# Kernel optimization log

Measured on AMD Instinct MI355X. Metric: run time of the kernel, lower is better.

The kernel has to match this reference:

```python
import jax, jax.numpy as jnp
import numpy as np
from jax import lax
jax.config.update("jax_enable_x64", True)

FNV_OFF = np.int64(-3750763034362895579)
FNV_PRIME = np.int64(4294967731)
I64_MAX = np.iinfo(np.int64).max
INF = np.float32(1e38)
CHUNK = 512  # cluster-chunk size for the cdist fallback


def _pack_key(b, c, vx, vy, vz):
    # five-word FNV-1a 64-bit hash with natural int64 wraparound
    h = jnp.full(b.shape, FNV_OFF, dtype=jnp.int64)
    for w in (b, c, vx, vy, vz):
        h = (h ^ w.astype(jnp.int64)) * FNV_PRIME
    return h


def _safe_norm(x):
    s = jnp.sum(x * x, axis=1)
    n = jnp.sqrt(jnp.where(s > 0, s, 1.0))
    return jnp.where(s > 0, n, 0.0)


def setup_inputs() -> dict:
    key = jax.random.key(0)
    k1, k2, k3, k4 = jax.random.split(key, 4)
    N = 65536
    grid = jax.random.randint(k1, (N, 3), 0, 400).astype(jnp.float32)
    batch_id = jnp.sort(jax.random.randint(k2, (N,), 0, 2).astype(jnp.int64))
    label = jax.random.randint(k3, (N,), 0, 8).astype(jnp.int64)
    pred_off = jax.random.normal(k4, (N, 3), dtype=jnp.float32)
    return {"pred_off": pred_off, "grid": grid, "label": label, "batch_id": batch_id,
            "base_grid": 16, "num_cls": 8, "num_batch": 2}


def _forward(pred_off, grid, label, batch_id, base_grid, num_cls, num_batch):
    N = grid.shape[0]
    grid_f = grid.astype(jnp.float32)
    vox = jnp.floor(grid_f / base_grid).astype(jnp.int64)  # [N,3]

    # voxel_grid: bucket by (batch, voxel) -> consecutive cluster ids via unique
    ckey = ((batch_id * 1024 + vox[:, 0]) * 1024 + vox[:, 1]) * 1024 + vox[:, 2]
    _, cluster = jnp.unique(ckey, return_inverse=True, size=N, fill_value=I64_MAX)
    cluster = cluster.reshape(-1)

    # cluster stats (segment scatter-reduce, num_segments = N upper bound)
    cnt = jax.ops.segment_sum(jnp.ones((N,), jnp.float32), cluster, num_segments=N)
    cl_center = jax.ops.segment_sum(grid_f, cluster, num_segments=N) / jnp.maximum(cnt, 1.0)[:, None]
    cl_batch = jax.ops.segment_min(batch_id, cluster, num_segments=N)
    cl_lbl_lo = jax.ops.segment_min(label, cluster, num_segments=N)
    cl_lbl_hi = jax.ops.segment_max(label, cluster, num_segments=N)
    cl_vox = jax.ops.segment_min(vox, cluster, num_segments=N)
    valid_cl = cnt > 0
    pure_cl = (cl_lbl_lo == cl_lbl_hi) & valid_cl
    pure_pt = pure_cl[cluster]

    # hash table of pure clusters, sorted by key (invalid -> sentinel, sorts last)
    pk_all = jnp.where(pure_cl, _pack_key(cl_batch, cl_lbl_lo, cl_vox[:, 0], cl_vox[:, 1], cl_vox[:, 2]), I64_MAX)
    order = jnp.argsort(pk_all)
    pk_sort = pk_all[order]
    pc_sort = cl_center[order]
    ok_sort = pure_cl[order]

    # per (batch,label) global centers
    key_bl = batch_id * num_cls + label
    nbl = num_batch * num_cls
    cnt_bl = jax.ops.segment_sum(jnp.ones((N,), jnp.float32), key_bl, num_segments=nbl)
    global_c = jax.ops.segment_sum(grid_f, key_bl, num_segments=nbl) / jnp.maximum(cnt_bl, 1.0)[:, None]
    step_sign = jnp.sign(global_c[key_bl] - cl_center[cluster]).astype(jnp.int64)  # [N,3]

    # +/-1 and +/-2 voxel hash lookup (steps 1 and K+1=2)
    def probe(step):
        cv = cl_vox[cluster] + step_sign * step
        ck = _pack_key(batch_id, label, cv[:, 0], cv[:, 1], cv[:, 2])
        idx = jnp.searchsorted(pk_sort, ck)
        idxc = jnp.minimum(idx, N - 1)
        hit = (idx < N) & ok_sort[idxc] & (pk_sort[idxc] == ck)
        return hit, pc_sort[idxc]

    hit1, t1 = probe(1)
    hit2, t2 = probe(2)
    hit_pt = hit1 | hit2
    tgt_c = jnp.where(hit1[:, None], t1, jnp.where(hit2[:, None], t2, grid_f))

    # fallback: nearest pure-cluster center with same (batch,label), chunked cdist+argmin
    miss = (~pure_pt) & (~hit_pt)
    code_y = key_bl
    code_x = jnp.where(pure_cl, cl_batch * num_cls + cl_lbl_lo, jnp.int64(-1))
    p2 = jnp.sum(grid_f * grid_f, axis=1)  # [N]

    def body(carry, i):
        best_d, best_c = carry
        c = lax.dynamic_slice_in_dim(cl_center, i * CHUNK, CHUNK)   # [S,3]
        cc = lax.dynamic_slice_in_dim(code_x, i * CHUNK, CHUNK)      # [S]
        d2 = p2[:, None] - 2.0 * (grid_f @ c.T) + jnp.sum(c * c, axis=1)[None, :]  # [N,S]
        d2 = jnp.where(cc[None, :] == code_y[:, None], d2, INF)
        j = jnp.argmin(d2, axis=1)
        dmin = jnp.take_along_axis(d2, j[:, None], axis=1)[:, 0]
        upd = dmin < best_d
        best_d = jnp.where(upd, dmin, best_d)
        best_c = jnp.where(upd[:, None], c[j], best_c)
        return (best_d, best_c), None

    nchunk = N // CHUNK
    (best_d, best_c), _ = lax.scan(body, (jnp.full((N,), INF, jnp.float32), grid_f), jnp.arange(nchunk))
    tgt_c = jnp.where((miss & (best_d < INF))[:, None], best_c, tgt_c)

    # loss: smooth-L1 on offsets below 99th-percentile magnitude + direction cosine loss
    tgt_off = tgt_c - grid_f
    mag = _safe_norm(tgt_off)
    thresh = jnp.quantile(mag, 0.99)
    m1 = mag <= thresh
    d = pred_off - tgt_off
    ad = jnp.abs(d)
    hub = jnp.where(ad < 1.0, 0.5 * d * d, ad - 0.5)
    n1 = jnp.sum(m1).astype(jnp.float32)
    loss_l1 = jnp.where(n1 > 0, jnp.sum(hub * m1[:, None]) / jnp.maximum(n1 * 3.0, 1.0), 0.0)

    md = (mag > 0) & m1
    eps = 1e-4
    pn = _safe_norm(pred_off)
    cos = jnp.sum(pred_off * tgt_off, axis=1) / jnp.maximum(pn * mag, eps)
    nmd = jnp.sum(md).astype(jnp.float32)
    loss_dir = jnp.where(nmd > 0, 1.0 - jnp.sum(cos * md) / jnp.maximum(nmd, 1.0), 0.0)
    return jnp.stack([loss_l1.astype(jnp.float32), loss_dir.astype(jnp.float32)])


def reference(pred_off, grid, label, batch_id, base_grid, num_cls, num_batch):
    return _forward(pred_off, grid, label, batch_id, base_grid, num_cls, num_batch)
```

## Files before the change

kernel.cpp:

```cpp
#include <hip/hip_runtime.h>
#include <climits>

#define VOXD 25
#define SLOT3 (VOXD*VOXD*VOXD)
#define SLOTS (2*SLOT3)
#define NCLS 8
#define NCODE 16
#define NBLK ((SLOTS + 255) / 256)
#define HB 2048
#define FPC 16
#define TILE 1024
#define CSTRIDE SLOT3

struct Scalars {
  double hub;
  double cosSum;
  int n1;
  int nmd;
  float thresh;
  int done;
  int done2;
};

__device__ __forceinline__ int voxslot(int b, int vx, int vy, int vz) {
  return ((b * VOXD + vx) * VOXD + vy) * VOXD + vz;
}

__device__ __forceinline__ int block_scan256(int v, int* ws) {
  int lane = threadIdx.x & 63, w = threadIdx.x >> 6;
  int s = v;
  #pragma unroll
  for (int off = 1; off < 64; off <<= 1) {
    int t = __shfl_up(s, off, 64);
    if (lane >= off) s += t;
  }
  if (lane == 63) ws[w] = s;
  __syncthreads();
  int add = 0;
  #pragma unroll
  for (int q = 0; q < 4; ++q) if (q < w) add += ws[q];
  __syncthreads();
  return s + add;
}

__global__ void k_scatter(const float* __restrict__ grid, const int* __restrict__ label,
                          const int* __restrict__ batch,
                          unsigned long long* vA, unsigned long long* vB, int* lmask,
                          int* blCnt, float* blSum, int n) {
  __shared__ int sCnt[NCODE];
  __shared__ float sSum[3 * NCODE];
  int tid = threadIdx.x;
  if (tid < NCODE) sCnt[tid] = 0;
  if (tid < 3 * NCODE) sSum[tid] = 0.f;
  __syncthreads();
  int i = blockIdx.x * blockDim.x + tid;
  if (i < n) {
    float gx = grid[3*i], gy = grid[3*i+1], gz = grid[3*i+2];
    int ix = (int)gx, iy = (int)gy, iz = (int)gz;
    int vx = (int)floorf(gx * (1.0f/16.0f));
    int vy = (int)floorf(gy * (1.0f/16.0f));
    int vz = (int)floorf(gz * (1.0f/16.0f));
    int b = batch[i], l = label[i];
    int s = voxslot(b, vx, vy, vz);
    atomicAdd(&vA[s], ((unsigned long long)(unsigned)ix << 32) | (unsigned)iy);
    atomicAdd(&vB[s], ((unsigned long long)(unsigned)iz << 24) | 1ULL);
    atomicOr(&lmask[s], 1 << l);
    int bl = b * NCLS + l;
    atomicAdd(&sCnt[bl], 1);
    atomicAdd(&sSum[3*bl], gx); atomicAdd(&sSum[3*bl+1], gy); atomicAdd(&sSum[3*bl+2], gz);
  }
  __syncthreads();
  if (tid < NCODE && sCnt[tid] != 0) atomicAdd(&blCnt[tid], sCnt[tid]);
  if (tid < 3 * NCODE && sSum[tid] != 0.f) atomicAdd(&blSum[tid], sSum[tid]);
}

__global__ void k_prep(const unsigned long long* vA, const unsigned long long* vB,
                       const int* lmask, float4* ctr, float4* pC, int* codeCnt) {
  __shared__ int lc[NCODE];
  __shared__ int lb[NCODE];
  int tid = threadIdx.x;
  if (tid < NCODE) lc[tid] = 0;
  __syncthreads();
  int s = blockIdx.x * 256 + tid;
  int code = -1, lpos = 0;
  float4 v = make_float4(0.f, 0.f, 0.f, __int_as_float(-2));
  if (s < SLOTS) {
    unsigned long long bq = vB[s];
    unsigned c = (unsigned)(bq & 0xFFFFFFULL);
    if (c > 0) {
      unsigned long long aq = vA[s];
      float fc = (float)c;
      float cx = __fdiv_rn((float)(unsigned)(aq >> 32), fc);
      float cy = __fdiv_rn((float)(unsigned)(aq & 0xFFFFFFFFULL), fc);
      float cz = __fdiv_rn((float)(unsigned)(bq >> 24), fc);
      int m = lmask[s];
      bool pure = (m & (m - 1)) == 0;
      int lbl = __ffs(m) - 1;
      v = make_float4(cx, cy, cz, __int_as_float(pure ? lbl : -1));
      if (pure) {
        code = (s / SLOT3) * NCLS + lbl;
        lpos = atomicAdd(&lc[code], 1);
      }
    }
    ctr[s] = v;
  }
  __syncthreads();
  if (tid < NCODE) lb[tid] = (lc[tid] > 0) ? atomicAdd(&codeCnt[tid], lc[tid]) : 0;
  __syncthreads();
  if (code >= 0) {
    int pos = code * CSTRIDE + lb[code] + lpos;
    pC[pos] = make_float4(v.x, v.y, v.z, __int_as_float(s));
  }
}

__global__ void k_targets(const float* __restrict__ grid, const int* __restrict__ label,
                          const int* __restrict__ batch,
                          const float4* __restrict__ ctr,
                          const int* __restrict__ blCnt, const float* __restrict__ blSum,
                          float* tgt, float* mag, int* ghist,
                          int* missPart, int* missCnt, int mstride, int n) {
  __shared__ int wCnt[4][NCODE];
  __shared__ int gBase[NCODE];
  __shared__ int h[HB];
  int tid = threadIdx.x, lane = tid & 63, w = tid >> 6;
  for (int t = tid; t < HB; t += 256) h[t] = 0;
  __syncthreads();
  int i = blockIdx.x * blockDim.x + tid;
  bool active = (i < n);
  bool miss = false;
  int mcode = -1;

  if (active) {
    float gx = grid[3*i], gy = grid[3*i+1], gz = grid[3*i+2];
    int vx = (int)floorf(gx * (1.0f/16.0f));
    int vy = (int)floorf(gy * (1.0f/16.0f));
    int vz = (int)floorf(gz * (1.0f/16.0f));
    int b = batch[i], l = label[i];
    int s = voxslot(b, vx, vy, vz);

    float4 own = ctr[s];
    bool purept = (__float_as_int(own.w) >= 0);

    int bl = b * NCLS + l;
    float fbc = (float)max(blCnt[bl], 1);
    float gcx = __fdiv_rn(blSum[3*bl],   fbc);
    float gcy = __fdiv_rn(blSum[3*bl+1], fbc);
    float gcz = __fdiv_rn(blSum[3*bl+2], fbc);

    float dx = __fsub_rn(gcx, own.x);
    float dy = __fsub_rn(gcy, own.y);
    float dz = __fsub_rn(gcz, own.z);
    int sgx = (dx > 0.f) ? 1 : ((dx < 0.f) ? -1 : 0);
    int sgy = (dy > 0.f) ? 1 : ((dy < 0.f) ? -1 : 0);
    int sgz = (dz > 0.f) ? 1 : ((dz < 0.f) ? -1 : 0);

    int ax1 = vx + sgx,     ay1 = vy + sgy,     az1 = vz + sgz;
    int ax2 = vx + 2 * sgx, ay2 = vy + 2 * sgy, az2 = vz + 2 * sgz;
    bool v1 = (unsigned)ax1 < (unsigned)VOXD && (unsigned)ay1 < (unsigned)VOXD &&
              (unsigned)az1 < (unsigned)VOXD;
    bool v2 = (unsigned)ax2 < (unsigned)VOXD && (unsigned)ay2 < (unsigned)VOXD &&
              (unsigned)az2 < (unsigned)VOXD;

    float4 q1 = make_float4(0.f, 0.f, 0.f, __int_as_float(-3));
    float4 q2 = q1;
    if (v1) q1 = ctr[voxslot(b, ax1, ay1, az1)];
    if (v2) q2 = ctr[voxslot(b, ax2, ay2, az2)];

    bool hit1 = v1 && (__float_as_int(q1.w) == l);
    bool hit2 = v2 && (__float_as_int(q2.w) == l);
    bool hit = hit1 || hit2;

    float tx = hit1 ? q1.x : (hit2 ? q2.x : gx);
    float ty = hit1 ? q1.y : (hit2 ? q2.y : gy);
    float tz = hit1 ? q1.z : (hit2 ? q2.z : gz);

    tgt[3*i] = tx; tgt[3*i+1] = ty; tgt[3*i+2] = tz;
    miss = (!purept && !hit);
    if (miss) {
      mcode = bl;
    } else {
      float tox = __fsub_rn(tx, gx), toy = __fsub_rn(ty, gy), toz = __fsub_rn(tz, gz);
      float ssq = __fadd_rn(__fadd_rn(__fmul_rn(tox,tox), __fmul_rn(toy,toy)),
                            __fmul_rn(toz,toz));
      float m = (ssq > 0.f) ? sqrtf(ssq) : 0.f;
      mag[i] = m;
      atomicAdd(&h[__float_as_uint(m) >> 21], 1);
    }
  }
  int myrank = 0;
  #pragma unroll
  for (int c = 0; c < NCODE; ++c) {
    unsigned long long mb = __ballot(mcode == c);
    if (lane == 0) wCnt[w][c] = __popcll(mb);
    if (mcode == c) myrank = __popcll(mb & ((1ULL << lane) - 1ULL));
  }
  __syncthreads();
  if (tid < NCODE) {
    int tot = wCnt[0][tid] + wCnt[1][tid] + wCnt[2][tid] + wCnt[3][tid];
    gBase[tid] = (tot > 0) ? atomicAdd(&missCnt[tid], tot) : 0;
  }
  __syncthreads();
  if (miss) {
    int base = gBase[mcode];
    for (int q = 0; q < 4; ++q) if (q < w) base += wCnt[q][mcode];
    missPart[mcode * mstride + base + myrank] = i;
  }
  for (int t = tid; t < HB; t += 256) {
    int c = h[t];
    if (c != 0) atomicAdd(&ghist[t], c);
  }
}

__global__ void __launch_bounds__(256) k_fallback(
    const float* __restrict__ grid,
    const float4* __restrict__ pC,
    const float4* __restrict__ ctr,
    const int* __restrict__ codeCnt,
    const int* __restrict__ missPart, const int* __restrict__ missCnt,
    float* tgt, float* mag, int* ghist, int mstride) {
  __shared__ float4 tile4[TILE];
  __shared__ int h[HB];
  int tid = threadIdx.x;
  int c = blockIdx.x / FPC;
  int y = blockIdx.x % FPC;
  int mc = missCnt[c];

  for (int t = tid; t < HB; t += 256) h[t] = 0;
  __syncthreads();

  if (y * 256 < mc) {
    int cc = codeCnt[c];
    int j0 = c * CSTRIDE;
    const int* mlist = missPart + c * mstride;
    for (int t0 = y * 256; t0 < mc; t0 += FPC * 256) {
      int t = t0 + tid;
      bool valid = (t < mc);
      int idx = 0;
      float gx = 0.f, gy = 0.f, gz = 0.f, p2 = 0.f;
      if (valid) {
        idx = mlist[t];
        gx = grid[3*idx]; gy = grid[3*idx+1]; gz = grid[3*idx+2];
        p2 = __fadd_rn(__fadd_rn(__fmul_rn(gx,gx), __fmul_rn(gy,gy)),
                       __fmul_rn(gz,gz));
      }
      unsigned long long key = 0xFFFFFFFFFFFFFFFFULL;
      for (int tb = 0; tb < cc; tb += TILE) {
        int m = min(TILE, cc - tb);
        __syncthreads();
        for (int j = tid; j < m; j += 256) tile4[j] = pC[j0 + tb + j];
        __syncthreads();
        #pragma unroll 4
        for (int j = 0; j < m; ++j) {
          float4 cl = tile4[j];
          float c2 = __fadd_rn(__fadd_rn(__fmul_rn(cl.x,cl.x), __fmul_rn(cl.y,cl.y)),
                               __fmul_rn(cl.z,cl.z));
          float dot = __fadd_rn(__fadd_rn(__fmul_rn(gx,cl.x), __fmul_rn(gy,cl.y)),
                                __fmul_rn(gz,cl.z));
          float d2 = __fadd_rn(__fsub_rn(p2, __fmul_rn(2.0f, dot)), c2);
          unsigned fb = __float_as_uint(d2);
          fb = (fb >> 31) ? ~fb : (fb | 0x80000000u);
          unsigned long long k2 = ((unsigned long long)fb << 32) |
                                  (unsigned)__float_as_int(cl.w);
          if (k2 < key) key = k2;
        }
      }
      if (valid) {
        float mv = 0.f;
        if (cc > 0) {
          int slot = (int)(unsigned)(key & 0xFFFFFFFFULL);
          float4 cl = ctr[slot];
          tgt[3*idx] = cl.x; tgt[3*idx+1] = cl.y; tgt[3*idx+2] = cl.z;
          float tox = __fsub_rn(cl.x, gx), toy = __fsub_rn(cl.y, gy),
                toz = __fsub_rn(cl.z, gz);
          float ssq = __fadd_rn(__fadd_rn(__fmul_rn(tox,tox), __fmul_rn(toy,toy)),
                                __fmul_rn(toz,toz));
          mv = (ssq > 0.f) ? sqrtf(ssq) : 0.f;
        }
        mag[idx] = mv;
        atomicAdd(&h[__float_as_uint(mv) >> 21], 1);
      }
    }
  }
  __syncthreads();
  for (int t = tid; t < HB; t += 256) {
    int cv = h[t];
    if (cv != 0) atomicAdd(&ghist[t], cv);
  }
}

__global__ void __launch_bounds__(256) k_loss_sel(
    const float* __restrict__ pred, const float* __restrict__ grid,
    const float* __restrict__ tgt, const float* __restrict__ mag,
    const int* __restrict__ ghist, uint2* defer, int* uCnt,
    Scalars* sc, float* out, int n, int nblocks, int r0, int r1, double tfrac) {
  __shared__ int h[HB];
  __shared__ int h2[HB];
  __shared__ int ws[4];
  __shared__ int s_misc[8];
  __shared__ double shH[256];
  __shared__ double shC[256];
  __shared__ int shN[256];
  __shared__ int shM[256];
  __shared__ int sLast;
  __shared__ float sTh;
  int tid = threadIdx.x, lane = tid & 63;

  int base8 = tid * 8;
  {
    int cbin[8];
    int s = 0;
    #pragma unroll
    for (int k = 0; k < 8; ++k) { cbin[k] = ghist[base8 + k]; s += cbin[k]; }
    int incl = block_scan256(s, ws);
    int lo = incl - s;
    if (r0 >= lo && r0 < lo + s) {
      int acc = lo;
      #pragma unroll
      for (int k = 0; k < 8; ++k) {
        if (r0 < acc + cbin[k]) { s_misc[0] = base8 + k; s_misc[1] = r0 - acc; break; }
        acc += cbin[k];
      }
    }
    if (r1 >= lo && r1 < lo + s) {
      int acc = lo;
      #pragma unroll
      for (int k = 0; k < 8; ++k) {
        if (r1 < acc + cbin[k]) { s_misc[2] = base8 + k; s_misc[3] = r1 - acc; break; }
        acc += cbin[k];
      }
    }
  }
  __syncthreads();
  int binA = s_misc[0], rA = s_misc[1], binB = s_misc[2], rB = s_misc[3];

  int i = blockIdx.x * 256 + tid;
  double hub = 0.0, cs = 0.0;
  int c1 = 0, cmd = 0;
  bool dfr = false;
  unsigned bits = 0;
  if (i < n) {
    float m = mag[i];
    bits = __float_as_uint(m);
    int cb = (int)(bits >> 21);
    if (cb == binA || cb == binB) {
      dfr = true;
    } else if (cb < binA) {
      c1 = 1;
      float tox = __fsub_rn(tgt[3*i],   grid[3*i]);
      float toy = __fsub_rn(tgt[3*i+1], grid[3*i+1]);
      float toz = __fsub_rn(tgt[3*i+2], grid[3*i+2]);
      float px = pred[3*i], py = pred[3*i+1], pz = pred[3*i+2];
      float d0 = __fsub_rn(px, tox), d1 = __fsub_rn(py, toy), d2 = __fsub_rn(pz, toz);
      float a0 = fabsf(d0), a1 = fabsf(d1), a2 = fabsf(d2);
      float h0 = (a0 < 1.f) ? __fmul_rn(__fmul_rn(0.5f, d0), d0) : __fsub_rn(a0, 0.5f);
      float h1 = (a1 < 1.f) ? __fmul_rn(__fmul_rn(0.5f, d1), d1) : __fsub_rn(a1, 0.5f);
      float h2v = (a2 < 1.f) ? __fmul_rn(__fmul_rn(0.5f, d2), d2) : __fsub_rn(a2, 0.5f);
      hub = (double)h0 + (double)h1 + (double)h2v;
      if (m > 0.f) {
        cmd = 1;
        float ps = __fadd_rn(__fadd_rn(__fmul_rn(px,px), __fmul_rn(py,py)), __fmul_rn(pz,pz));
        float pn = (ps > 0.f) ? sqrtf(ps) : 0.f;
        float dotp = __fadd_rn(__fadd_rn(__fmul_rn(px,tox), __fmul_rn(py,toy)),
                               __fmul_rn(pz,toz));
        float den = fmaxf(__fmul_rn(pn, m), 1e-4f);
        cs = (double)__fdiv_rn(dotp, den);
      }
    }
  }
  {
    unsigned long long mb = __ballot(dfr);
    int mcp = __popcll(mb);
    int bs = 0;
    if (lane == 0 && mcp > 0) bs = atomicAdd(uCnt, mcp);
    bs = __shfl(bs, 0, 64);
    if (dfr) defer[bs + __popcll(mb & ((1ULL << lane) - 1ULL))] =
        make_uint2(bits, (unsigned)i);
  }
  shH[tid] = hub; shC[tid] = cs; shN[tid] = c1; shM[tid] = cmd;
  __syncthreads();
  for (int off = 128; off > 0; off >>= 1) {
    if (tid < off) {
      shH[tid] += shH[tid+off];
      shC[tid] += shC[tid+off];
      shN[tid] += shN[tid+off];
      shM[tid] += shM[tid+off];
    }
    __syncthreads();
  }
  if (tid == 0) {
    atomicAdd(&sc->hub, shH[0]);
    atomicAdd(&sc->cosSum, shC[0]);
    atomicAdd(&sc->n1, shN[0]);
    atomicAdd(&sc->nmd, shM[0]);
    __threadfence();
    int d = atomicAdd(&sc->done2, 1);
    sLast = (d == nblocks - 1) ? 1 : 0;
  }
  __syncthreads();
  if (!sLast) return;
  __threadfence();

  int U = atomicAdd(uCnt, 0);

  for (int t = tid; t < HB; t += 256) { h[t] = 0; h2[t] = 0; }
  __syncthreads();
  for (int t = tid; t < U; t += 256) {
    unsigned v = defer[t].x;
    int cb = (int)(v >> 21);
    if (cb == binA) atomicAdd(&h[(v >> 10) & 0x7FF], 1);
    if (cb == binB) atomicAdd(&h2[(v >> 10) & 0x7FF], 1);
  }
  __syncthreads();
  {
    int a8[8], sA = 0;
    #pragma unroll
    for (int k = 0; k < 8; ++k) { a8[k] = h[base8 + k]; sA += a8[k]; }
    int inclA = block_scan256(sA, ws);
    int accA = inclA - sA;
    #pragma unroll
    for (int k = 0; k < 8; ++k) {
      if (rA >= accA && rA < accA + a8[k]) { s_misc[4] = base8 + k; s_misc[5] = rA - accA; }
      accA += a8[k];
    }
    int b8[8], sB = 0;
    #pragma unroll
    for (int k = 0; k < 8; ++k) { b8[k] = h2[base8 + k]; sB += b8[k]; }
    int inclB = block_scan256(sB, ws);
    int accB = inclB - sB;
    #pragma unroll
    for (int k = 0; k < 8; ++k) {
      if (rB >= accB && rB < accB + b8[k]) { s_misc[6] = base8 + k; s_misc[7] = rB - accB; }
      accB += b8[k];
    }
  }
  __syncthreads();
  int subA = s_misc[4], subRA = s_misc[5], subB = s_misc[6], subRB = s_misc[7];

  for (int t = tid; t < 1024; t += 256) { h[t] = 0; h2[t] = 0; }
  __syncthreads();
  for (int t = tid; t < U; t += 256) {
    unsigned v = defer[t].x;
    int cb = (int)(v >> 21);
    if (cb == binA && (int)((v >> 10) & 0x7FF) == subA) atomicAdd(&h[v & 0x3FF], 1);
    if (cb == binB && (int)((v >> 10) & 0x7FF) == subB) atomicAdd(&h2[v & 0x3FF], 1);
  }
  __syncthreads();
  {
    int base4 = tid * 4;
    int la[4], sA = 0;
    #pragma unroll
    for (int k = 0; k < 4; ++k) { la[k] = h[base4 + k]; sA += la[k]; }
    int inclA = block_scan256(sA, ws);
    int accA = inclA - sA;
    #pragma unroll
    for (int k = 0; k < 4; ++k) {
      if (subRA >= accA && subRA < accA + la[k]) s_misc[0] = base4 + k;
      accA += la[k];
    }
    int lb4[4], sB = 0;
    #pragma unroll
    for (int k = 0; k < 4; ++k) { lb4[k] = h2[base4 + k]; sB += lb4[k]; }
    int inclB = block_scan256(sB, ws);
    int accB = inclB - sB;
    #pragma unroll
    for (int k = 0; k < 4; ++k) {
      if (subRB >= accB && subRB < accB + lb4[k]) s_misc[1] = base4 + k;
      accB += lb4[k];
    }
  }
  __syncthreads();
  if (tid == 0) {
    unsigned va = ((unsigned)binA << 21) | ((unsigned)subA << 10) | (unsigned)s_misc[0];
    unsigned vb = ((unsigned)binB << 21) | ((unsigned)subB << 10) | (unsigned)s_misc[1];
    double a = (double)__uint_as_float(va);
    double b = (double)__uint_as_float(vb);
    double th = (tfrac >= 0.5) ? (b - (b - a) * (1.0 - tfrac)) : (a + (b - a) * tfrac);
    sc->thresh = (float)th;
    sTh = (float)th;
  }
  __syncthreads();
  float th = sTh;

  double hub2 = 0.0, cs2 = 0.0;
  int c12 = 0, cmd2 = 0;
  for (int t = tid; t < U; t += 256) {
    uint2 e = defer[t];
    float m = __uint_as_float(e.x);
    if (m <= th) {
      int idx = (int)e.y;
      c12 += 1;
      float tox = __fsub_rn(tgt[3*idx],   grid[3*idx]);
      float toy = __fsub_rn(tgt[3*idx+1], grid[3*idx+1]);
      float toz = __fsub_rn(tgt[3*idx+2], grid[3*idx+2]);
      float px = pred[3*idx], py = pred[3*idx+1], pz = pred[3*idx+2];
      float d0 = __fsub_rn(px, tox), d1 = __fsub_rn(py, toy), d2 = __fsub_rn(pz, toz);
      float a0 = fabsf(d0), a1 = fabsf(d1), a2 = fabsf(d2);
      float h0 = (a0 < 1.f) ? __fmul_rn(__fmul_rn(0.5f, d0), d0) : __fsub_rn(a0, 0.5f);
      float h1 = (a1 < 1.f) ? __fmul_rn(__fmul_rn(0.5f, d1), d1) : __fsub_rn(a1, 0.5f);
      float h2v = (a2 < 1.f) ? __fmul_rn(__fmul_rn(0.5f, d2), d2) : __fsub_rn(a2, 0.5f);
      hub2 += (double)h0 + (double)h1 + (double)h2v;
      if (m > 0.f) {
        cmd2 += 1;
        float ps = __fadd_rn(__fadd_rn(__fmul_rn(px,px), __fmul_rn(py,py)), __fmul_rn(pz,pz));
        float pn = (ps > 0.f) ? sqrtf(ps) : 0.f;
        float dotp = __fadd_rn(__fadd_rn(__fmul_rn(px,tox), __fmul_rn(py,toy)),
                               __fmul_rn(pz,toz));
        float den = fmaxf(__fmul_rn(pn, m), 1e-4f);
        cs2 += (double)__fdiv_rn(dotp, den);
      }
    }
  }
  shH[tid] = hub2; shC[tid] = cs2; shN[tid] = c12; shM[tid] = cmd2;
  __syncthreads();
  for (int off = 128; off > 0; off >>= 1) {
    if (tid < off) {
      shH[tid] += shH[tid+off];
      shC[tid] += shC[tid+off];
      shN[tid] += shN[tid+off];
      shM[tid] += shM[tid+off];
    }
    __syncthreads();
  }
  if (tid == 0) {
    double th_hub = atomicAdd(&sc->hub, 0.0) + shH[0];
    double th_cos = atomicAdd(&sc->cosSum, 0.0) + shC[0];
    int n1 = atomicAdd(&sc->n1, 0) + shN[0];
    int nmd = atomicAdd(&sc->nmd, 0) + shM[0];
    double l1 = (n1 > 0) ? th_hub / fmax((double)n1 * 3.0, 1.0) : 0.0;
    double ld = (nmd > 0) ? (1.0 - th_cos / fmax((double)nmd, 1.0)) : 0.0;
    out[0] = (float)l1;
    out[1] = (float)ld;
  }
}

extern "C" void kernel_launch(void* const* d_in, const int* in_sizes, int n_in,
                              void* d_out, int out_size, void* d_ws, size_t ws_size,
                              hipStream_t stream) {
  const float* pred  = (const float*)d_in[0];
  const float* grid  = (const float*)d_in[1];
  const int*   label = (const int*)d_in[2];
  const int*   batch = (const int*)d_in[3];
  int n = in_sizes[2];
  int mstride = n / 4;

  char* p = (char*)d_ws;
  auto take = [&](size_t bytes) -> char* {
    char* r = p;
    p += (bytes + 255) & ~(size_t)255;
    return r;
  };
  char* zbase = p;
  unsigned long long* vA = (unsigned long long*)take((size_t)SLOTS*8);
  unsigned long long* vB = (unsigned long long*)take((size_t)SLOTS*8);
  int*    lmask    = (int*)   take((size_t)SLOTS*4);
  int*    codeCnt  = (int*)   take(NCODE*4);
  int*    missCnt  = (int*)   take(NCODE*4);
  int*    blCnt    = (int*)   take(16*4);
  float*  blSum    = (float*) take(48*4);
  int*    ghist    = (int*)   take((size_t)HB*4);
  int*    uCnt     = (int*)   take(4);
  Scalars* sc      = (Scalars*)take(sizeof(Scalars));
  size_t zbytes = (size_t)(p - zbase);
  float4* ctr      = (float4*)take((size_t)SLOTS*16);
  float4* pC       = (float4*)take((size_t)NCODE*CSTRIDE*16);
  float*  tgt      = (float*) take((size_t)n*3*4);
  float*  mag      = (float*) take((size_t)n*4);
  int*    missPart = (int*)   take((size_t)NCODE*mstride*4);
  uint2*  defer    = (uint2*) take((size_t)n*8);

  int nb = (n + 255) / 256;
  int nfb = NCODE * FPC;

  double vi = 0.99 * (double)(n - 1);
  int r0 = (int)vi;
  int r1 = r0 + 1; if (r1 > n - 1) r1 = n - 1;
  double tfrac = vi - (double)r0;

  hipMemsetAsync(zbase, 0, zbytes, stream);
  k_scatter<<<nb, 256, 0, stream>>>(grid, label, batch, vA, vB, lmask,
                                    blCnt, blSum, n);
  k_prep<<<NBLK, 256, 0, stream>>>(vA, vB, lmask, ctr, pC, codeCnt);
  k_targets<<<nb, 256, 0, stream>>>(grid, label, batch, ctr, blCnt, blSum,
                                    tgt, mag, ghist, missPart, missCnt, mstride, n);
  k_fallback<<<nfb, 256, 0, stream>>>(grid, pC, ctr, codeCnt,
                                      missPart, missCnt, tgt, mag, ghist, mstride);
  k_loss_sel<<<nb, 256, 0, stream>>>(pred, grid, tgt, mag, ghist, defer, uCnt,
                                     sc, (float*)d_out, n, nb, r0, r1, tfrac);
}
```

Measured before the change: 161.3 us.

## Split fallback cluster scan across warps per query and precompute center norms

The brute-force nearest-cluster fallback now assigns 64 query points per block instead of 256. The four wavefronts each scan a strided quarter of the cluster tile, and their packed keys are min-reduced through shared memory. This launches four times as many blocks and spreads the long per-point cluster loop over more of the GPU. The squared norm of each cluster center is computed once when the tile is loaded rather than by every thread, and the per-block shared histogram is replaced with direct global atomics. The cost is extra block-level synchronisation per query batch and more global atomic traffic on the histogram.

```diff
diff --git a/kernel.cpp b/kernel.cpp
--- a/kernel.cpp
+++ b/kernel.cpp
@@ -8,7 +8,7 @@
 #define NCODE 16
 #define NBLK ((SLOTS + 255) / 256)
 #define HB 2048
-#define FPC 16
+#define BPC 64
 #define TILE 1024
 #define CSTRIDE SLOT3
 
@@ -219,72 +219,77 @@
     const int* __restrict__ missPart, const int* __restrict__ missCnt,
     float* tgt, float* mag, int* ghist, int mstride) {
   __shared__ float4 tile4[TILE];
-  __shared__ int h[HB];
-  int tid = threadIdx.x;
-  int c = blockIdx.x / FPC;
-  int y = blockIdx.x % FPC;
+  __shared__ int    stile[TILE];
+  __shared__ unsigned long long bkeyw[4][64];
+  int tid = threadIdx.x, lane = tid & 63, w = tid >> 6;
+  int c = blockIdx.x / BPC;
+  int y = blockIdx.x % BPC;
   int mc = missCnt[c];
-
-  for (int t = tid; t < HB; t += 256) h[t] = 0;
-  __syncthreads();
-
-  if (y * 256 < mc) {
-    int cc = codeCnt[c];
-    int j0 = c * CSTRIDE;
-    const int* mlist = missPart + c * mstride;
-    for (int t0 = y * 256; t0 < mc; t0 += FPC * 256) {
-      int t = t0 + tid;
-      bool valid = (t < mc);
-      int idx = 0;
-      float gx = 0.f, gy = 0.f, gz = 0.f, p2 = 0.f;
-      if (valid) {
-        idx = mlist[t];
-        gx = grid[3*idx]; gy = grid[3*idx+1]; gz = grid[3*idx+2];
-        p2 = __fadd_rn(__fadd_rn(__fmul_rn(gx,gx), __fmul_rn(gy,gy)),
-                       __fmul_rn(gz,gz));
-      }
-      unsigned long long key = 0xFFFFFFFFFFFFFFFFULL;
-      for (int tb = 0; tb < cc; tb += TILE) {
-        int m = min(TILE, cc - tb);
-        __syncthreads();
-        for (int j = tid; j < m; j += 256) tile4[j] = pC[j0 + tb + j];
-        __syncthreads();
-        #pragma unroll 4
-        for (int j = 0; j < m; ++j) {
-          float4 cl = tile4[j];
-          float c2 = __fadd_rn(__fadd_rn(__fmul_rn(cl.x,cl.x), __fmul_rn(cl.y,cl.y)),
-                               __fmul_rn(cl.z,cl.z));
-          float dot = __fadd_rn(__fadd_rn(__fmul_rn(gx,cl.x), __fmul_rn(gy,cl.y)),
-                                __fmul_rn(gz,cl.z));
-          float d2 = __fadd_rn(__fsub_rn(p2, __fmul_rn(2.0f, dot)), c2);
-          unsigned fb = __float_as_uint(d2);
-          fb = (fb >> 31) ? ~fb : (fb | 0x80000000u);
-          unsigned long long k2 = ((unsigned long long)fb << 32) |
-                                  (unsigned)__float_as_int(cl.w);
-          if (k2 < key) key = k2;
-        }
-      }
-      if (valid) {
-        float mv = 0.f;
-        if (cc > 0) {
-          int slot = (int)(unsigned)(key & 0xFFFFFFFFULL);
-          float4 cl = ctr[slot];
-          tgt[3*idx] = cl.x; tgt[3*idx+1] = cl.y; tgt[3*idx+2] = cl.z;
-          float tox = __fsub_rn(cl.x, gx), toy = __fsub_rn(cl.y, gy),
-                toz = __fsub_rn(cl.z, gz);
-          float ssq = __fadd_rn(__fadd_rn(__fmul_rn(tox,tox), __fmul_rn(toy,toy)),
-                                __fmul_rn(toz,toz));
-          mv = (ssq > 0.f) ? sqrtf(ssq) : 0.f;
-        }
-        mag[idx] = mv;
-        atomicAdd(&h[__float_as_uint(mv) >> 21], 1);
-      }
-    }
-  }
-  __syncthreads();
-  for (int t = tid; t < HB; t += 256) {
-    int cv = h[t];
-    if (cv != 0) atomicAdd(&ghist[t], cv);
+  if (y * 64 >= mc) return;
+  int cc = codeCnt[c];
+  int j0 = c * CSTRIDE;
+  const int* mlist = missPart + c * mstride;
+
+  for (int t0 = y * 64; t0 < mc; t0 += BPC * 64) {
+    int t = t0 + lane;
+    bool valid = (t < mc);
+    int idx = 0;
+    float gx = 0.f, gy = 0.f, gz = 0.f, p2 = 0.f;
+    if (valid) {
+      idx = mlist[t];
+      gx = grid[3*idx]; gy = grid[3*idx+1]; gz = grid[3*idx+2];
+      p2 = __fadd_rn(__fadd_rn(__fmul_rn(gx,gx), __fmul_rn(gy,gy)),
+                     __fmul_rn(gz,gz));
+    }
+    unsigned long long key = 0xFFFFFFFFFFFFFFFFULL;
+    for (int tb = 0; tb < cc; tb += TILE) {
+      int m = min(TILE, cc - tb);
+      __syncthreads();
+      for (int j = tid; j < m; j += 256) {
+        float4 cl = pC[j0 + tb + j];
+        float c2 = __fadd_rn(__fadd_rn(__fmul_rn(cl.x,cl.x), __fmul_rn(cl.y,cl.y)),
+                             __fmul_rn(cl.z,cl.z));
+        tile4[j] = make_float4(cl.x, cl.y, cl.z, c2);
+        stile[j] = __float_as_int(cl.w);
+      }
+      __syncthreads();
+      #pragma unroll 4
+      for (int j = w; j < m; j += 4) {
+        float4 cl = tile4[j];
+        float dot = __fadd_rn(__fadd_rn(__fmul_rn(gx,cl.x), __fmul_rn(gy,cl.y)),
+                              __fmul_rn(gz,cl.z));
+        float d2 = __fadd_rn(__fsub_rn(p2, __fmul_rn(2.0f, dot)), cl.w);
+        unsigned fb = __float_as_uint(d2);
+        fb = (fb >> 31) ? ~fb : (fb | 0x80000000u);
+        unsigned long long k2 = ((unsigned long long)fb << 32) | (unsigned)stile[j];
+        if (k2 < key) key = k2;
+      }
+    }
+    bkeyw[w][lane] = key;
+    __syncthreads();
+    if (w == 0 && valid) {
+      unsigned long long k0 = bkeyw[0][lane];
+      unsigned long long k1 = bkeyw[1][lane];
+      unsigned long long k2_ = bkeyw[2][lane];
+      unsigned long long k3 = bkeyw[3][lane];
+      unsigned long long kk = k0 < k1 ? k0 : k1;
+      unsigned long long kh = k2_ < k3 ? k2_ : k3;
+      if (kh < kk) kk = kh;
+      float mv = 0.f;
+      if (cc > 0) {
+        int slot = (int)(unsigned)(kk & 0xFFFFFFFFULL);
+        float4 cl = ctr[slot];
+        tgt[3*idx] = cl.x; tgt[3*idx+1] = cl.y; tgt[3*idx+2] = cl.z;
+        float tox = __fsub_rn(cl.x, gx), toy = __fsub_rn(cl.y, gy),
+              toz = __fsub_rn(cl.z, gz);
+        float ssq = __fadd_rn(__fadd_rn(__fmul_rn(tox,tox), __fmul_rn(toy,toy)),
+                              __fmul_rn(toz,toz));
+        mv = (ssq > 0.f) ? sqrtf(ssq) : 0.f;
+      }
+      mag[idx] = mv;
+      atomicAdd(&ghist[__float_as_uint(mv) >> 21], 1);
+    }
+    __syncthreads();
   }
 }
 
@@ -569,7 +574,7 @@
   uint2*  defer    = (uint2*) take((size_t)n*8);
 
   int nb = (n + 255) / 256;
-  int nfb = NCODE * FPC;
+  int nfb = NCODE * BPC;
 
   double vi = 0.99 * (double)(n - 1);
   int r0 = (int)vi;
```

After: 308.4 us. 91.2% more time.
